# Performance work log

Measured on AMD Instinct MI355X. Metric: run time of the kernel, lower is better.

## Reference

```python
import jax, jax.numpy as jnp
import numpy as np
from math import sqrt

EMBED_DIM = 1024
PROJ_DIM = 128
BATCH = 4
SEQ = 4096


def setup_inputs() -> dict:
    key = jax.random.key(0)
    ks = jax.random.split(key, 7)
    x = jax.random.normal(ks[0], (BATCH, SEQ, EMBED_DIM), dtype=jnp.float32)
    # nn.Linear default init scale ~ 1/sqrt(fan_in); use small random weights
    s_e = 1.0 / sqrt(EMBED_DIM)
    Wq = jax.random.uniform(ks[1], (EMBED_DIM, PROJ_DIM), jnp.float32, -s_e, s_e)
    bq = jax.random.uniform(ks[2], (PROJ_DIM,), jnp.float32, -s_e, s_e)
    Wk = jax.random.uniform(ks[3], (EMBED_DIM, PROJ_DIM), jnp.float32, -s_e, s_e)
    bk = jax.random.uniform(ks[4], (PROJ_DIM,), jnp.float32, -s_e, s_e)
    Wov = jax.random.uniform(ks[5], (EMBED_DIM, EMBED_DIM), jnp.float32, -s_e, s_e)
    bov = jax.random.uniform(ks[6], (EMBED_DIM,), jnp.float32, -s_e, s_e)
    return {"x": x, "Wq": Wq, "bq": bq, "Wk": Wk, "bk": bk, "Wov": Wov, "bov": bov}


def reference(x, Wq, bq, Wk, bk, Wov, bov):
    # q, k: (b, s, p); ov: (b, s, d)
    queries = jnp.einsum('bse,ep->bsp', x, Wq) + bq
    keys = jnp.einsum('bse,ep->bsp', x, Wk) + bk
    scores = jnp.einsum('bqp,bkp->bqk', queries, keys) / sqrt(PROJ_DIM)
    pattern = jax.nn.softmax(scores, axis=-1)
    ov = jnp.einsum('bse,ed->bsd', x, Wov) + bov
    return jnp.einsum('bqk,bkd->bqd', pattern, ov)
```

## Files before the change

kernel.cpp:

```cpp
#include <hip/hip_runtime.h>
#include <hip/hip_bf16.h>

#define BATCH 4
#define SEQ   4096
#define EMB   1024
#define PDIM  128

using short8   = __attribute__((ext_vector_type(8))) short;
using ushort8  = __attribute__((ext_vector_type(8))) unsigned short;
using ushort4v = __attribute__((ext_vector_type(4))) unsigned short;
using float4v  = __attribute__((ext_vector_type(4))) float;

__device__ __forceinline__ unsigned short f2bf(float f) {
  union { float f; unsigned int u; } x; x.f = f;
  unsigned int r = x.u + 0x7fffu + ((x.u >> 16) & 1u);
  return (unsigned short)(r >> 16);
}
__device__ __forceinline__ float bf2f(unsigned short u) {
  union { unsigned int u; float f; } x; x.u = ((unsigned int)u) << 16;
  return x.f;
}

__device__ __forceinline__ void gld_lds16(const unsigned short* g, unsigned short* l) {
  __builtin_amdgcn_global_load_lds(
      (__attribute__((address_space(1))) void*)(g),
      (__attribute__((address_space(3))) void*)(l), 16, 0, 0);
}

__global__ void cast_bf16_kernel(const float* __restrict__ src,
                                 unsigned short* __restrict__ dst, int n4) {
  int i = blockIdx.x * blockDim.x + threadIdx.x;
  if (i >= n4) return;
  float4v v = ((const float4v*)src)[i];
  ushort4v o;
  o[0] = f2bf(v[0]); o[1] = f2bf(v[1]); o[2] = f2bf(v[2]); o[3] = f2bf(v[3]);
  ((ushort4v*)dst)[i] = o;
}

__global__ void transpose_cast_kernel(const float* __restrict__ src,
                                      unsigned short* __restrict__ dst, int R, int C) {
  __shared__ float tile[32][33];
  const float* s = src + (size_t)blockIdx.z * R * C;
  unsigned short* d = dst + (size_t)blockIdx.z * R * C;
  int c0 = blockIdx.x * 32, r0 = blockIdx.y * 32;
#pragma unroll
  for (int i = 0; i < 32; i += 8)
    tile[threadIdx.y + i][threadIdx.x] =
        s[(size_t)(r0 + threadIdx.y + i) * C + c0 + threadIdx.x];
  __syncthreads();
#pragma unroll
  for (int i = 0; i < 32; i += 8)
    d[(size_t)(c0 + threadIdx.y + i) * R + r0 + threadIdx.x] =
        f2bf(tile[threadIdx.x][threadIdx.y + i]);
}

__global__ void concat_bias_kernel(const float* __restrict__ a,
                                   const float* __restrict__ b,
                                   float* __restrict__ o) {
  int i = threadIdx.x;
  o[i] = (i < PDIM) ? a[i] : b[i - PDIM];
}

__global__ __launch_bounds__(256, 2) void gemm_kernel(
    const unsigned short* __restrict__ A, int lda, size_t saz,
    const unsigned short* __restrict__ Bt, int ldb, size_t sbz,
    void* __restrict__ Cv, int ldc, size_t scz,
    int K, const float* __restrict__ bias,
    const float* __restrict__ rowscale, int srz,
    float scale, int mode) {
  __shared__ __attribute__((aligned(16))) unsigned short As[128 * 32];
  __shared__ __attribute__((aligned(16))) unsigned short Bs[128 * 32];
  const int tid = threadIdx.x;
  const int wave = tid >> 6, lane = tid & 63;
  const int quad = lane >> 4, l16 = lane & 15;
  const int m0 = blockIdx.x * 128, n0 = blockIdx.y * 128;
  const int z = blockIdx.z;
  const int mq = (wave >> 1) * 64, nq = (wave & 1) * 64;

  A  += (size_t)z * saz;
  Bt += (size_t)z * sbz;

  const int c0 = wave * 2, c1 = wave * 2 + 1;
  const int r0 = c0 * 16 + (lane >> 2), r1 = c1 * 16 + (lane >> 2);
  const int koff = (lane & 3) * 8;
  const unsigned short* Ag0 = A + (size_t)(m0 + r0) * lda + koff;
  const unsigned short* Ag1 = A + (size_t)(m0 + r1) * lda + koff;
  const unsigned short* Bg0 = Bt + (size_t)(n0 + r0) * ldb + koff;
  const unsigned short* Bg1 = Bt + (size_t)(n0 + r1) * ldb + koff;
  unsigned short* Al0 = As + c0 * 16 * 32;
  unsigned short* Al1 = As + c1 * 16 * 32;
  unsigned short* Bl0 = Bs + c0 * 16 * 32;
  unsigned short* Bl1 = Bs + c1 * 16 * 32;

  float4v zf = {0.f, 0.f, 0.f, 0.f};
  float4v acc[4][4];
#pragma unroll
  for (int i = 0; i < 4; i++)
#pragma unroll
    for (int j = 0; j < 4; j++) acc[i][j] = zf;

  for (int k0 = 0; k0 < K; k0 += 32) {
    if (k0) __syncthreads();
    gld_lds16(Ag0 + k0, Al0);
    gld_lds16(Ag1 + k0, Al1);
    gld_lds16(Bg0 + k0, Bl0);
    gld_lds16(Bg1 + k0, Bl1);
    __syncthreads();

    short8 af[4], bf[4];
#pragma unroll
    for (int t = 0; t < 4; t++) {
      af[t] = *(const short8*)(As + (mq + t * 16 + l16) * 32 + quad * 8);
      bf[t] = *(const short8*)(Bs + (nq + t * 16 + l16) * 32 + quad * 8);
    }
#pragma unroll
    for (int mt = 0; mt < 4; mt++)
#pragma unroll
      for (int nt = 0; nt < 4; nt++)
        acc[mt][nt] = __builtin_amdgcn_mfma_f32_16x16x32_bf16(af[mt], bf[nt], acc[mt][nt], 0, 0, 0);
  }

  float* Cf = (float*)Cv + (size_t)z * scz;
  unsigned short* Cb = (unsigned short*)Cv + (size_t)z * scz;
  const float* rs = rowscale ? rowscale + (size_t)z * srz : nullptr;

#pragma unroll
  for (int mt = 0; mt < 4; mt++)
#pragma unroll
    for (int nt = 0; nt < 4; nt++) {
      int gn = n0 + nq + nt * 16 + l16;
      float bv = (mode == 0 || mode == 3) ? bias[gn] : 0.f;
#pragma unroll
      for (int r = 0; r < 4; r++) {
        int gm = m0 + mq + mt * 16 + quad * 4 + r;
        float v = acc[mt][nt][r];
        if (mode == 0)      Cf[(size_t)gm * ldc + gn] = v + bv;
        else if (mode == 1) Cb[(size_t)gm * ldc + gn] = f2bf(__expf(v * scale));
        else if (mode == 2) Cb[(size_t)gm * ldc + gn] = f2bf(v * rs[gm]);
        else                Cb[(size_t)gm * ldc + gn] = f2bf(v + bv);
      }
    }
}

__global__ void rowsum_kernel(const unsigned short* __restrict__ P,
                              float* __restrict__ linv, int N) {
  const int row = blockIdx.x, b = blockIdx.y, tid = threadIdx.x;
  const unsigned short* p = P + (size_t)b * SEQ * SEQ + (size_t)row * N;
  float s = 0.f;
  for (int i = tid * 8; i < N; i += 256 * 8) {
    ushort8 v = *(const ushort8*)(p + i);
#pragma unroll
    for (int j = 0; j < 8; j++) s += bf2f(v[j]);
  }
#pragma unroll
  for (int o = 32; o > 0; o >>= 1) s += __shfl_down(s, o);
  __shared__ float rs[4];
  if ((tid & 63) == 0) rs[tid >> 6] = s;
  __syncthreads();
  if (tid == 0) linv[(size_t)b * SEQ + row] = 1.f / (rs[0] + rs[1] + rs[2] + rs[3]);
}

extern "C" void kernel_launch(void* const* d_in, const int* in_sizes, int n_in,
                              void* d_out, int out_size, void* d_ws, size_t ws_size,
                              hipStream_t stream) {
  const float* x   = (const float*)d_in[0];
  const float* Wq  = (const float*)d_in[1];
  const float* bq  = (const float*)d_in[2];
  const float* Wk  = (const float*)d_in[3];
  const float* bk  = (const float*)d_in[4];
  const float* Wov = (const float*)d_in[5];
  const float* bov = (const float*)d_in[6];
  float* out = (float*)d_out;

  char* ws = (char*)d_ws;
  size_t off = 0;
  auto alloc = [&](size_t bytes) {
    char* p = ws + off;
    off += (bytes + 255) & ~(size_t)255;
    return p;
  };
  const int M = BATCH * SEQ;
  unsigned short* x_bf = (unsigned short*)alloc((size_t)M * EMB * 2);
  unsigned short* xT   = (unsigned short*)alloc((size_t)M * EMB * 2);
  unsigned short* WqkT = (unsigned short*)alloc((size_t)2 * PDIM * EMB * 2);
  unsigned short* WovT = (unsigned short*)alloc((size_t)EMB * EMB * 2);
  float*          bqk  = (float*)alloc(2 * PDIM * sizeof(float));
  unsigned short* qk   = (unsigned short*)alloc((size_t)M * 2 * PDIM * 2);
  float*          linv = (float*)alloc((size_t)M * sizeof(float));
  unsigned short* ctx  = (unsigned short*)alloc((size_t)M * EMB * 2);
  const size_t pslot = (size_t)SEQ * SEQ * 2;
  unsigned short* P = (unsigned short*)(ws + off);
  size_t rem = ws_size > off ? ws_size - off : 0;
  int g = (rem >= 4 * pslot) ? 4 : (rem >= 2 * pslot) ? 2 : 1;

  cast_bf16_kernel<<<(M * EMB / 4 + 255) / 256, 256, 0, stream>>>(x, x_bf, M * EMB / 4);
  transpose_cast_kernel<<<dim3(EMB / 32, SEQ / 32, BATCH), dim3(32, 8), 0, stream>>>(x, xT, SEQ, EMB);
  transpose_cast_kernel<<<dim3(PDIM / 32, EMB / 32, 1), dim3(32, 8), 0, stream>>>(Wq, WqkT, EMB, PDIM);
  transpose_cast_kernel<<<dim3(PDIM / 32, EMB / 32, 1), dim3(32, 8), 0, stream>>>(Wk, WqkT + (size_t)PDIM * EMB, EMB, PDIM);
  transpose_cast_kernel<<<dim3(EMB / 32, EMB / 32, 1), dim3(32, 8), 0, stream>>>(Wov, WovT, EMB, EMB);
  concat_bias_kernel<<<1, 256, 0, stream>>>(bq, bk, bqk);

  gemm_kernel<<<dim3(M / 128, 2, 1), 256, 0, stream>>>(
      x_bf, EMB, 0, WqkT, EMB, 0, qk, 2 * PDIM, 0, EMB, bqk, nullptr, 0, 1.f, 3);

  const float qscale = 0.08838834764831845f;
  for (int b0 = 0; b0 < BATCH; b0 += g) {
    int gg = (b0 + g <= BATCH) ? g : (BATCH - b0);
    gemm_kernel<<<dim3(SEQ / 128, SEQ / 128, gg), 256, 0, stream>>>(
        qk + (size_t)b0 * SEQ * 2 * PDIM, 2 * PDIM, (size_t)SEQ * 2 * PDIM,
        qk + (size_t)b0 * SEQ * 2 * PDIM + PDIM, 2 * PDIM, (size_t)SEQ * 2 * PDIM,
        P, SEQ, (size_t)SEQ * SEQ,
        PDIM, nullptr, nullptr, 0, qscale, 1);
    rowsum_kernel<<<dim3(SEQ, gg), 256, 0, stream>>>(P, linv + (size_t)b0 * SEQ, SEQ);
    gemm_kernel<<<dim3(SEQ / 128, EMB / 128, gg), 256, 0, stream>>>(
        P, SEQ, (size_t)SEQ * SEQ,
        xT + (size_t)b0 * EMB * SEQ, SEQ, (size_t)EMB * SEQ,
        ctx + (size_t)b0 * SEQ * EMB, EMB, (size_t)SEQ * EMB,
        SEQ, nullptr, linv + (size_t)b0 * SEQ, SEQ, 1.f, 2);
  }

  gemm_kernel<<<dim3(M / 128, EMB / 128, 1), 256, 0, stream>>>(
      ctx, EMB, 0, WovT, EMB, 0, out, EMB, 0, EMB, bov, nullptr, 0, 1.f, 0);
}
```

Before: 478.3 us.

## Fuse softmax rowsum into score GEMM, swizzle LDS, widen N tiles, merge x prep

The score GEMM epilogue now accumulates row sums of the exponentials and adds them atomically into a zeroed buffer, which removes the separate rowsum pass that re-read the full probability matrix. The GEMM is templated on N tile width, with 128x256 tiles for the large GEMMs, and uses an XOR swizzle on the LDS layout to reduce bank conflicts. The bf16 cast and transpose of x are merged into one kernel. Risks are more accumulator registers per wave at the 256-wide tile, nondeterministic float atomics, and summing fp32 exponentials instead of their bf16-rounded values.

```diff
diff --git a/kernel.cpp b/kernel.cpp
--- a/kernel.cpp
+++ b/kernel.cpp
@@ -8,7 +8,6 @@
 
 using short8   = __attribute__((ext_vector_type(8))) short;
 using ushort8  = __attribute__((ext_vector_type(8))) unsigned short;
-using ushort4v = __attribute__((ext_vector_type(4))) unsigned short;
 using float4v  = __attribute__((ext_vector_type(4))) float;
 
 __device__ __forceinline__ unsigned short f2bf(float f) {
@@ -16,10 +15,6 @@
   unsigned int r = x.u + 0x7fffu + ((x.u >> 16) & 1u);
   return (unsigned short)(r >> 16);
 }
-__device__ __forceinline__ float bf2f(unsigned short u) {
-  union { unsigned int u; float f; } x; x.u = ((unsigned int)u) << 16;
-  return x.f;
-}
 
 __device__ __forceinline__ void gld_lds16(const unsigned short* g, unsigned short* l) {
   __builtin_amdgcn_global_load_lds(
@@ -27,30 +22,39 @@
       (__attribute__((address_space(3))) void*)(l), 16, 0, 0);
 }
 
-__global__ void cast_bf16_kernel(const float* __restrict__ src,
-                                 unsigned short* __restrict__ dst, int n4) {
-  int i = blockIdx.x * blockDim.x + threadIdx.x;
-  if (i >= n4) return;
-  float4v v = ((const float4v*)src)[i];
-  ushort4v o;
-  o[0] = f2bf(v[0]); o[1] = f2bf(v[1]); o[2] = f2bf(v[2]); o[3] = f2bf(v[3]);
-  ((ushort4v*)dst)[i] = o;
+__global__ void xprep_kernel(const float* __restrict__ src,
+                             unsigned short* __restrict__ rm,
+                             unsigned short* __restrict__ tp, int R, int C) {
+  __shared__ float tile[32][33];
+  const float* s = src + (size_t)blockIdx.z * R * C;
+  unsigned short* drm = rm + (size_t)blockIdx.z * R * C;
+  unsigned short* dtp = tp + (size_t)blockIdx.z * R * C;
+  int c0 = blockIdx.x * 32, r0 = blockIdx.y * 32;
+#pragma unroll
+  for (int i = 0; i < 32; i += 8) {
+    float v = s[(size_t)(r0 + threadIdx.y + i) * C + c0 + threadIdx.x];
+    tile[threadIdx.y + i][threadIdx.x] = v;
+    drm[(size_t)(r0 + threadIdx.y + i) * C + c0 + threadIdx.x] = f2bf(v);
+  }
+  __syncthreads();
+#pragma unroll
+  for (int i = 0; i < 32; i += 8)
+    dtp[(size_t)(c0 + threadIdx.y + i) * R + r0 + threadIdx.x] =
+        f2bf(tile[threadIdx.x][threadIdx.y + i]);
 }
 
 __global__ void transpose_cast_kernel(const float* __restrict__ src,
                                       unsigned short* __restrict__ dst, int R, int C) {
   __shared__ float tile[32][33];
-  const float* s = src + (size_t)blockIdx.z * R * C;
-  unsigned short* d = dst + (size_t)blockIdx.z * R * C;
   int c0 = blockIdx.x * 32, r0 = blockIdx.y * 32;
 #pragma unroll
   for (int i = 0; i < 32; i += 8)
     tile[threadIdx.y + i][threadIdx.x] =
-        s[(size_t)(r0 + threadIdx.y + i) * C + c0 + threadIdx.x];
+        src[(size_t)(r0 + threadIdx.y + i) * C + c0 + threadIdx.x];
   __syncthreads();
 #pragma unroll
   for (int i = 0; i < 32; i += 8)
-    d[(size_t)(c0 + threadIdx.y + i) * R + r0 + threadIdx.x] =
+    dst[(size_t)(c0 + threadIdx.y + i) * R + r0 + threadIdx.x] =
         f2bf(tile[threadIdx.x][threadIdx.y + i]);
 }
 
@@ -61,103 +65,148 @@
   o[i] = (i < PDIM) ? a[i] : b[i - PDIM];
 }
 
+template <int NT>
 __global__ __launch_bounds__(256, 2) void gemm_kernel(
     const unsigned short* __restrict__ A, int lda, size_t saz,
     const unsigned short* __restrict__ Bt, int ldb, size_t sbz,
     void* __restrict__ Cv, int ldc, size_t scz,
     int K, const float* __restrict__ bias,
-    const float* __restrict__ rowscale, int srz,
+    float* __restrict__ lsum, int slz,
     float scale, int mode) {
+  constexpr int NW = NT / 32;
+  constexpr int BC = NT / 64;
   __shared__ __attribute__((aligned(16))) unsigned short As[128 * 32];
-  __shared__ __attribute__((aligned(16))) unsigned short Bs[128 * 32];
+  __shared__ __attribute__((aligned(16))) unsigned short Bs[NT * 32];
   const int tid = threadIdx.x;
   const int wave = tid >> 6, lane = tid & 63;
   const int quad = lane >> 4, l16 = lane & 15;
-  const int m0 = blockIdx.x * 128, n0 = blockIdx.y * 128;
+  const int m0 = blockIdx.x * 128, n0 = blockIdx.y * NT;
   const int z = blockIdx.z;
-  const int mq = (wave >> 1) * 64, nq = (wave & 1) * 64;
+  const int mq = (wave >> 1) * 64, nq = (wave & 1) * (NT / 2);
 
   A  += (size_t)z * saz;
   Bt += (size_t)z * sbz;
 
-  const int c0 = wave * 2, c1 = wave * 2 + 1;
-  const int r0 = c0 * 16 + (lane >> 2), r1 = c1 * 16 + (lane >> 2);
-  const int koff = (lane & 3) * 8;
-  const unsigned short* Ag0 = A + (size_t)(m0 + r0) * lda + koff;
-  const unsigned short* Ag1 = A + (size_t)(m0 + r1) * lda + koff;
-  const unsigned short* Bg0 = Bt + (size_t)(n0 + r0) * ldb + koff;
-  const unsigned short* Bg1 = Bt + (size_t)(n0 + r1) * ldb + koff;
-  unsigned short* Al0 = As + c0 * 16 * 32;
-  unsigned short* Al1 = As + c1 * 16 * 32;
-  unsigned short* Bl0 = Bs + c0 * 16 * 32;
-  unsigned short* Bl1 = Bs + c1 * 16 * 32;
+  const int lr = lane >> 2;
+  const int koff = (((lane & 3) ^ ((lane >> 3) & 3)) << 3);
+  const unsigned short* Ag[2];
+  unsigned short* Al[2];
+#pragma unroll
+  for (int j = 0; j < 2; j++) {
+    int c = wave * 2 + j;
+    Ag[j] = A + (size_t)(m0 + c * 16 + lr) * lda + koff;
+    Al[j] = As + c * 512;
+  }
+  const unsigned short* Bg[BC];
+  unsigned short* Bl[BC];
+#pragma unroll
+  for (int j = 0; j < BC; j++) {
+    int c = wave * BC + j;
+    Bg[j] = Bt + (size_t)(n0 + c * 16 + lr) * ldb + koff;
+    Bl[j] = Bs + c * 512;
+  }
 
   float4v zf = {0.f, 0.f, 0.f, 0.f};
-  float4v acc[4][4];
+  float4v acc[4][NW];
 #pragma unroll
   for (int i = 0; i < 4; i++)
 #pragma unroll
-    for (int j = 0; j < 4; j++) acc[i][j] = zf;
+    for (int j = 0; j < NW; j++) acc[i][j] = zf;
+
+  const int rsw = ((l16 >> 1) & 3);
 
   for (int k0 = 0; k0 < K; k0 += 32) {
     if (k0) __syncthreads();
-    gld_lds16(Ag0 + k0, Al0);
-    gld_lds16(Ag1 + k0, Al1);
-    gld_lds16(Bg0 + k0, Bl0);
-    gld_lds16(Bg1 + k0, Bl1);
+#pragma unroll
+    for (int j = 0; j < 2; j++) gld_lds16(Ag[j] + k0, Al[j]);
+#pragma unroll
+    for (int j = 0; j < BC; j++) gld_lds16(Bg[j] + k0, Bl[j]);
     __syncthreads();
 
-    short8 af[4], bf[4];
-#pragma unroll
-    for (int t = 0; t < 4; t++) {
-      af[t] = *(const short8*)(As + (mq + t * 16 + l16) * 32 + quad * 8);
-      bf[t] = *(const short8*)(Bs + (nq + t * 16 + l16) * 32 + quad * 8);
-    }
-#pragma unroll
-    for (int mt = 0; mt < 4; mt++)
-#pragma unroll
-      for (int nt = 0; nt < 4; nt++)
-        acc[mt][nt] = __builtin_amdgcn_mfma_f32_16x16x32_bf16(af[mt], bf[nt], acc[mt][nt], 0, 0, 0);
+    short8 af[4], bfr[NW];
+#pragma unroll
+    for (int t = 0; t < 4; t++)
+      af[t] = *(const short8*)(As + (mq + t * 16 + l16) * 32 + ((quad ^ rsw) << 3));
+#pragma unroll
+    for (int t = 0; t < NW; t++)
+      bfr[t] = *(const short8*)(Bs + (nq + t * 16 + l16) * 32 + ((quad ^ rsw) << 3));
+#pragma unroll
+    for (int mt = 0; mt < 4; mt++)
+#pragma unroll
+      for (int nt = 0; nt < NW; nt++)
+        acc[mt][nt] = __builtin_amdgcn_mfma_f32_16x16x32_bf16(af[mt], bfr[nt], acc[mt][nt], 0, 0, 0);
   }
 
   float* Cf = (float*)Cv + (size_t)z * scz;
   unsigned short* Cb = (unsigned short*)Cv + (size_t)z * scz;
-  const float* rs = rowscale ? rowscale + (size_t)z * srz : nullptr;
-
-#pragma unroll
-  for (int mt = 0; mt < 4; mt++)
-#pragma unroll
-    for (int nt = 0; nt < 4; nt++) {
-      int gn = n0 + nq + nt * 16 + l16;
-      float bv = (mode == 0 || mode == 3) ? bias[gn] : 0.f;
+
+  if (mode == 1) {
+    float rsum[4][4];
+#pragma unroll
+    for (int mt = 0; mt < 4; mt++)
+#pragma unroll
+      for (int r = 0; r < 4; r++) rsum[mt][r] = 0.f;
+#pragma unroll
+    for (int mt = 0; mt < 4; mt++)
+#pragma unroll
+      for (int nt = 0; nt < NW; nt++) {
+        int gn = n0 + nq + nt * 16 + l16;
+#pragma unroll
+        for (int r = 0; r < 4; r++) {
+          float e = __expf(acc[mt][nt][r] * scale);
+          Cb[(size_t)(m0 + mq + mt * 16 + quad * 4 + r) * ldc + gn] = f2bf(e);
+          rsum[mt][r] += e;
+        }
+      }
+#pragma unroll
+    for (int mt = 0; mt < 4; mt++)
 #pragma unroll
       for (int r = 0; r < 4; r++) {
-        int gm = m0 + mq + mt * 16 + quad * 4 + r;
-        float v = acc[mt][nt][r];
-        if (mode == 0)      Cf[(size_t)gm * ldc + gn] = v + bv;
-        else if (mode == 1) Cb[(size_t)gm * ldc + gn] = f2bf(__expf(v * scale));
-        else if (mode == 2) Cb[(size_t)gm * ldc + gn] = f2bf(v * rs[gm]);
-        else                Cb[(size_t)gm * ldc + gn] = f2bf(v + bv);
-      }
+        float s = rsum[mt][r];
+#pragma unroll
+        for (int o = 1; o < 16; o <<= 1) s += __shfl_xor(s, o);
+        rsum[mt][r] = s;
+      }
+    if (l16 == 0) {
+#pragma unroll
+      for (int mt = 0; mt < 4; mt++)
+#pragma unroll
+        for (int r = 0; r < 4; r++)
+          atomicAdd(&lsum[(size_t)z * slz + m0 + mq + mt * 16 + quad * 4 + r], rsum[mt][r]);
     }
-}
-
-__global__ void rowsum_kernel(const unsigned short* __restrict__ P,
-                              float* __restrict__ linv, int N) {
-  const int row = blockIdx.x, b = blockIdx.y, tid = threadIdx.x;
-  const unsigned short* p = P + (size_t)b * SEQ * SEQ + (size_t)row * N;
-  float s = 0.f;
-  for (int i = tid * 8; i < N; i += 256 * 8) {
-    ushort8 v = *(const ushort8*)(p + i);
-#pragma unroll
-    for (int j = 0; j < 8; j++) s += bf2f(v[j]);
-  }
-#pragma unroll
-  for (int o = 32; o > 0; o >>= 1) s += __shfl_down(s, o);
-  __shared__ float rs[4];
-  if ((tid & 63) == 0) rs[tid >> 6] = s;
-  __syncthreads();
-  if (tid == 0) linv[(size_t)b * SEQ + row] = 1.f / (rs[0] + rs[1] + rs[2] + rs[3]);
+  } else if (mode == 2) {
+    float linv[4][4];
+#pragma unroll
+    for (int mt = 0; mt < 4; mt++)
+#pragma unroll
+      for (int r = 0; r < 4; r++)
+        linv[mt][r] = 1.f / lsum[(size_t)z * slz + m0 + mq + mt * 16 + quad * 4 + r];
+#pragma unroll
+    for (int mt = 0; mt < 4; mt++)
+#pragma unroll
+      for (int nt = 0; nt < NW; nt++) {
+        int gn = n0 + nq + nt * 16 + l16;
+#pragma unroll
+        for (int r = 0; r < 4; r++)
+          Cb[(size_t)(m0 + mq + mt * 16 + quad * 4 + r) * ldc + gn] =
+              f2bf(acc[mt][nt][r] * linv[mt][r]);
+      }
+  } else {
+#pragma unroll
+    for (int mt = 0; mt < 4; mt++)
+#pragma unroll
+      for (int nt = 0; nt < NW; nt++) {
+        int gn = n0 + nq + nt * 16 + l16;
+        float bv = bias[gn];
+#pragma unroll
+        for (int r = 0; r < 4; r++) {
+          int gm = m0 + mq + mt * 16 + quad * 4 + r;
+          float v = acc[mt][nt][r] + bv;
+          if (mode == 0) Cf[(size_t)gm * ldc + gn] = v;
+          else           Cb[(size_t)gm * ldc + gn] = f2bf(v);
+        }
+      }
+  }
 }
 
 extern "C" void kernel_launch(void* const* d_in, const int* in_sizes, int n_in,
@@ -193,32 +242,31 @@
   size_t rem = ws_size > off ? ws_size - off : 0;
   int g = (rem >= 4 * pslot) ? 4 : (rem >= 2 * pslot) ? 2 : 1;
 
-  cast_bf16_kernel<<<(M * EMB / 4 + 255) / 256, 256, 0, stream>>>(x, x_bf, M * EMB / 4);
-  transpose_cast_kernel<<<dim3(EMB / 32, SEQ / 32, BATCH), dim3(32, 8), 0, stream>>>(x, xT, SEQ, EMB);
-  transpose_cast_kernel<<<dim3(PDIM / 32, EMB / 32, 1), dim3(32, 8), 0, stream>>>(Wq, WqkT, EMB, PDIM);
-  transpose_cast_kernel<<<dim3(PDIM / 32, EMB / 32, 1), dim3(32, 8), 0, stream>>>(Wk, WqkT + (size_t)PDIM * EMB, EMB, PDIM);
-  transpose_cast_kernel<<<dim3(EMB / 32, EMB / 32, 1), dim3(32, 8), 0, stream>>>(Wov, WovT, EMB, EMB);
+  xprep_kernel<<<dim3(EMB / 32, SEQ / 32, BATCH), dim3(32, 8), 0, stream>>>(x, x_bf, xT, SEQ, EMB);
+  transpose_cast_kernel<<<dim3(PDIM / 32, EMB / 32), dim3(32, 8), 0, stream>>>(Wq, WqkT, EMB, PDIM);
+  transpose_cast_kernel<<<dim3(PDIM / 32, EMB / 32), dim3(32, 8), 0, stream>>>(Wk, WqkT + (size_t)PDIM * EMB, EMB, PDIM);
+  transpose_cast_kernel<<<dim3(EMB / 32, EMB / 32), dim3(32, 8), 0, stream>>>(Wov, WovT, EMB, EMB);
   concat_bias_kernel<<<1, 256, 0, stream>>>(bq, bk, bqk);
-
-  gemm_kernel<<<dim3(M / 128, 2, 1), 256, 0, stream>>>(
+  hipMemsetAsync(linv, 0, M * sizeof(float), stream);
+
+  gemm_kernel<128><<<dim3(M / 128, 2, 1), 256, 0, stream>>>(
       x_bf, EMB, 0, WqkT, EMB, 0, qk, 2 * PDIM, 0, EMB, bqk, nullptr, 0, 1.f, 3);
 
   const float qscale = 0.08838834764831845f;
   for (int b0 = 0; b0 < BATCH; b0 += g) {
     int gg = (b0 + g <= BATCH) ? g : (BATCH - b0);
-    gemm_kernel<<<dim3(SEQ / 128, SEQ / 128, gg), 256, 0, stream>>>(
+    gemm_kernel<256><<<dim3(SEQ / 128, SEQ / 256, gg), 256, 0, stream>>>(
         qk + (size_t)b0 * SEQ * 2 * PDIM, 2 * PDIM, (size_t)SEQ * 2 * PDIM,
         qk + (size_t)b0 * SEQ * 2 * PDIM + PDIM, 2 * PDIM, (size_t)SEQ * 2 * PDIM,
         P, SEQ, (size_t)SEQ * SEQ,
-        PDIM, nullptr, nullptr, 0, qscale, 1);
-    rowsum_kernel<<<dim3(SEQ, gg), 256, 0, stream>>>(P, linv + (size_t)b0 * SEQ, SEQ);
-    gemm_kernel<<<dim3(SEQ / 128, EMB / 128, gg), 256, 0, stream>>>(
+        PDIM, nullptr, linv + (size_t)b0 * SEQ, SEQ, qscale, 1);
+    gemm_kernel<256><<<dim3(SEQ / 128, EMB / 256, gg), 256, 0, stream>>>(
         P, SEQ, (size_t)SEQ * SEQ,
         xT + (size_t)b0 * EMB * SEQ, SEQ, (size_t)EMB * SEQ,
         ctx + (size_t)b0 * SEQ * EMB, EMB, (size_t)SEQ * EMB,
         SEQ, nullptr, linv + (size_t)b0 * SEQ, SEQ, 1.f, 2);
   }
 
-  gemm_kernel<<<dim3(M / 128, EMB / 128, 1), 256, 0, stream>>>(
+  gemm_kernel<256><<<dim3(M / 128, EMB / 256, 1), 256, 0, stream>>>(
       ctx, EMB, 0, WovT, EMB, 0, out, EMB, 0, EMB, bov, nullptr, 0, 1.f, 0);
 }
```

Result: faster. 401.5 us (-16.1%).
